# Kernel tuning notes

Hardware: AMD Instinct MI355X
Metric: run time of the kernel (lower is better)

The kernel has to match this reference:

```python
import jax, jax.numpy as jnp
import numpy as np

NUM_HEADS = 16

def setup_inputs() -> dict:
    key = jax.random.key(0)
    k1, k2, k3 = jax.random.split(key, 3)
    B, S, D = 2, 2048, 1024
    return {
        "hidden_states": jax.random.normal(k1, (B, S, D), dtype=jnp.float32),
        "W_attn": jax.random.normal(k2, (D, 3 * D), dtype=jnp.float32) * 0.02,
        "b_attn": jnp.zeros((3 * D,), dtype=jnp.float32),
        "W_proj": jax.random.normal(k3, (D, D), dtype=jnp.float32) * 0.02,
        "b_proj": jnp.zeros((D,), dtype=jnp.float32),
    }

def reference(hidden_states, W_attn, b_attn, W_proj, b_proj):
    B, S, D = hidden_states.shape
    H = NUM_HEADS
    hd = D // H
    # qkv projection (Conv1D == addmm): [B,S,3D]
    qkv = hidden_states @ W_attn + b_attn
    q, k, v = jnp.split(qkv, 3, axis=-1)
    # split heads -> [B,H,S,hd]
    def split_heads(t):
        return t.reshape(B, S, H, hd).transpose(0, 2, 1, 3)
    q, k, v = split_heads(q), split_heads(k), split_heads(v)
    # scaled QK^T: [B,H,S,S]
    scores = jnp.einsum('bhqd,bhkd->bhqk', q, k) / jnp.asarray(hd ** 0.5, dtype=q.dtype)
    causal = jnp.tril(jnp.ones((S, S), dtype=bool))
    mask_value = jnp.finfo(scores.dtype).min
    scores = jnp.where(causal, scores, mask_value)
    probs = jax.nn.softmax(scores, axis=-1)  # attn_pdrop=0 -> no dropout
    out = jnp.einsum('bhqk,bhkd->bhqd', probs, v)
    # merge heads -> [B,S,D]
    out = out.transpose(0, 2, 1, 3).reshape(B, S, D)
    out = out @ W_proj + b_proj  # resid_pdrop=0 -> no dropout
    return out
```

## Files before the change

### kernel.cpp

```cpp
#include <hip/hip_runtime.h>
#include <math.h>

typedef __attribute__((ext_vector_type(8))) short bf16x8;
typedef __attribute__((ext_vector_type(4))) short bf16x4;
typedef __attribute__((ext_vector_type(4))) float f32x4;

#define MFMA16(a, b, c) __builtin_amdgcn_mfma_f32_16x16x32_bf16(a, b, c, 0, 0, 0)

#define GLOAD_LDS16(g, l)                                                        \
    __builtin_amdgcn_global_load_lds(                                            \
        (const __attribute__((address_space(1))) void*)(g),                      \
        (__attribute__((address_space(3))) void*)(l), 16, 0, 0)

__device__ __forceinline__ short f2bf(float f) {
    union { float f; unsigned u; } x; x.f = f;
    unsigned r = (x.u + 0x7fffu + ((x.u >> 16) & 1u)) >> 16;
    return (short)r;
}

__global__ __launch_bounds__(256) void convert_bf16_kernel(
    const float* __restrict__ in, short* __restrict__ out, int n4) {
    int i = blockIdx.x * 256 + threadIdx.x;
    if (i >= n4) return;
    float4 v = ((const float4*)in)[i];
    bf16x4 o;
    o[0] = f2bf(v.x); o[1] = f2bf(v.y); o[2] = f2bf(v.z); o[3] = f2bf(v.w);
    ((bf16x4*)out)[i] = o;
}

__global__ __launch_bounds__(256) void transpose_w2_kernel(
    const float* __restrict__ Wa, const float* __restrict__ Wp,
    short* __restrict__ WaT, short* __restrict__ WpT) {
    __shared__ float tile[32][33];
    const float* W; short* Wt; int N, xb;
    if (blockIdx.x < 96) { W = Wa; Wt = WaT; N = 3072; xb = blockIdx.x; }
    else                 { W = Wp; Wt = WpT; N = 1024; xb = blockIdx.x - 96; }
    const int K = 1024;
    int c = threadIdx.x & 31, r0 = threadIdx.x >> 5;
    int n0 = xb << 5, k0 = blockIdx.y << 5;
#pragma unroll
    for (int i = 0; i < 4; i++) {
        int r = r0 + i * 8;
        tile[r][c] = W[(long)(k0 + r) * N + n0 + c];
    }
    __syncthreads();
#pragma unroll
    for (int i = 0; i < 4; i++) {
        int r = r0 + i * 8;
        Wt[(long)(n0 + r) * K + k0 + c] = f2bf(tile[c][r]);
    }
}

__global__ __launch_bounds__(256) void gemm_qkv_kernel(
    const short* __restrict__ A, const short* __restrict__ Bt,
    const float* __restrict__ bias,
    short* __restrict__ QK, short* __restrict__ VTb, int Kdim) {
    __shared__ __align__(16) short lsAll[17408];
    short* lsA = lsAll;
    short* lsB = lsAll + 8192;
    const int tid = threadIdx.x;
    const int lane = tid & 63, l15 = lane & 15, quad = lane >> 4;
    const int w = tid >> 6, wm = w >> 1, wn = w & 1;
    const int m0 = blockIdx.y * 128, n0 = blockIdx.x * 128;
    const int e = l15 & 7;
    const int lrow = lane >> 3;
    const int lgcol = ((lane & 7) ^ lrow) << 3;

    f32x4 acc[4][4];
#pragma unroll
    for (int i = 0; i < 4; i++)
#pragma unroll
        for (int j = 0; j < 4; j++) acc[i][j] = (f32x4){0.f, 0.f, 0.f, 0.f};

    for (int k0 = 0; k0 < Kdim; k0 += 64) {
#pragma unroll
        for (int ii = 0; ii < 4; ii++) {
            const int i = (w << 2) + ii;
            const int grow = (i << 3) + lrow;
            GLOAD_LDS16(&A[(size_t)(m0 + grow) * Kdim + k0 + lgcol], &lsA[i * 512]);
            GLOAD_LDS16(&Bt[(size_t)(n0 + grow) * Kdim + k0 + lgcol], &lsB[i * 512]);
        }
        __syncthreads();
#pragma unroll
        for (int kk = 0; kk < 64; kk += 32) {
            const int kb = kk >> 3;
            bf16x8 af[4], bfr[4];
#pragma unroll
            for (int t = 0; t < 4; t++) {
                const int sw = (((kb + quad) ^ e) << 3);
                af[t] = *(const bf16x8*)&lsA[(wm * 64 + t * 16 + l15) * 64 + sw];
                bfr[t] = *(const bf16x8*)&lsB[(wn * 64 + t * 16 + l15) * 64 + sw];
            }
#pragma unroll
            for (int mt = 0; mt < 4; mt++)
#pragma unroll
                for (int nt = 0; nt < 4; nt++)
                    acc[mt][nt] = MFMA16(af[mt], bfr[nt], acc[mt][nt]);
        }
        __syncthreads();
    }

    if (n0 < 2048) {
        const float scale = (n0 < 1024) ? 0.18033688011112042f : 1.0f;
#pragma unroll
        for (int nt = 0; nt < 4; nt++) {
            int nn = n0 + wn * 64 + nt * 16 + l15;
            float bv = bias[nn];
#pragma unroll
            for (int mt = 0; mt < 4; mt++)
#pragma unroll
                for (int r = 0; r < 4; r++) {
                    int mm = m0 + wm * 64 + mt * 16 + quad * 4 + r;
                    QK[(long)mm * 2048 + nn] = f2bf((acc[mt][nt][r] + bv) * scale);
                }
        }
    } else {
        short* vt = &lsAll[w * (64 * 68)];
#pragma unroll
        for (int nt = 0; nt < 4; nt++) {
            int nn = n0 + wn * 64 + nt * 16 + l15;
            float bv = bias[nn];
#pragma unroll
            for (int mt = 0; mt < 4; mt++) {
                bf16x4 pk;
#pragma unroll
                for (int r = 0; r < 4; r++) pk[r] = f2bf(acc[mt][nt][r] + bv);
                *(bf16x4*)&vt[(nt * 16 + l15) * 68 + mt * 16 + quad * 4] = pk;
            }
        }
        const int hh = ((n0 - 2048) >> 6) + wn;
        const int bb = m0 >> 11;
        const int srow = (m0 & 2047) + wm * 64;
        const int sloc = (lane & 7) << 3;
#pragma unroll
        for (int i = 0; i < 8; i++) {
            const int d = i * 8 + (lane >> 3);
            bf16x8 vv = *(const bf16x8*)&vt[d * 68 + sloc];
            *(bf16x8*)&VTb[((size_t)(bb * 16 + hh) * 64 + d) * 2048 + srow + sloc] = vv;
        }
    }
}

__global__ __launch_bounds__(256) void gemm_proj_kernel(
    const short* __restrict__ A, const short* __restrict__ Bt,
    const float* __restrict__ bias, float* __restrict__ outF) {
    __shared__ __align__(16) short lsA[128 * 64];
    __shared__ __align__(16) short lsB[64 * 64];
    const int tid = threadIdx.x;
    const int lane = tid & 63, l15 = lane & 15, quad = lane >> 4, w = tid >> 6;
    const int m0 = blockIdx.y * 128, n0 = blockIdx.x * 64;
    const int e = l15 & 7;
    const int lrow = lane >> 3;
    const int lgcol = ((lane & 7) ^ lrow) << 3;

    f32x4 acc[2][4];
#pragma unroll
    for (int i = 0; i < 2; i++)
#pragma unroll
        for (int j = 0; j < 4; j++) acc[i][j] = (f32x4){0.f, 0.f, 0.f, 0.f};

    for (int k0 = 0; k0 < 1024; k0 += 64) {
#pragma unroll
        for (int ii = 0; ii < 4; ii++) {
            const int i = (w << 2) + ii;
            const int grow = (i << 3) + lrow;
            GLOAD_LDS16(&A[(size_t)(m0 + grow) * 1024 + k0 + lgcol], &lsA[i * 512]);
        }
#pragma unroll
        for (int ii = 0; ii < 2; ii++) {
            const int i = (w << 1) + ii;
            const int grow = (i << 3) + lrow;
            GLOAD_LDS16(&Bt[(size_t)(n0 + grow) * 1024 + k0 + lgcol], &lsB[i * 512]);
        }
        __syncthreads();
#pragma unroll
        for (int kk = 0; kk < 64; kk += 32) {
            const int kb = kk >> 3;
            const int sw = (((kb + quad) ^ e) << 3);
            bf16x8 af[2], bfr[4];
#pragma unroll
            for (int mt = 0; mt < 2; mt++)
                af[mt] = *(const bf16x8*)&lsA[(w * 32 + mt * 16 + l15) * 64 + sw];
#pragma unroll
            for (int nt = 0; nt < 4; nt++)
                bfr[nt] = *(const bf16x8*)&lsB[(nt * 16 + l15) * 64 + sw];
#pragma unroll
            for (int mt = 0; mt < 2; mt++)
#pragma unroll
                for (int nt = 0; nt < 4; nt++)
                    acc[mt][nt] = MFMA16(af[mt], bfr[nt], acc[mt][nt]);
        }
        __syncthreads();
    }

#pragma unroll
    for (int nt = 0; nt < 4; nt++) {
        int nn = n0 + nt * 16 + l15;
        float bv = bias[nn];
#pragma unroll
        for (int mt = 0; mt < 2; mt++)
#pragma unroll
            for (int r = 0; r < 4; r++) {
                int mm = m0 + w * 32 + mt * 16 + quad * 4 + r;
                outF[(long)mm * 1024 + nn] = acc[mt][nt][r] + bv;
            }
    }
}

__global__ __launch_bounds__(256, 4) void attn_kernel(
    const short* __restrict__ QK, const short* __restrict__ VT,
    short* __restrict__ Ao) {
    __shared__ __align__(16) short Kt[2][64 * 64];
    __shared__ __align__(16) short Vt[2][64 * 64];
    __shared__ __align__(16) short Pt[4][1024];
    const int tid = threadIdx.x;
    const int lane = tid & 63, l15 = lane & 15, quad = lane >> 4, w = tid >> 6;
    const int bx = blockIdx.x;
    const int qt = 31 - (bx >> 5);
    const int hb = bx & 31;
    const int b = hb >> 4, h = hb & 15;
    const size_t rowbase = (size_t)b * 2048 * 2048 + h * 64;
    const short* Qb = QK + rowbase;
    const short* Kb = QK + rowbase + 1024;
    const short* Vh = VT + (size_t)hb * 64 * 2048;
    short* Pw = &Pt[w][0];
    const int e = l15 & 7;

    const int srow0 = tid >> 3, sc40 = (tid & 7) ^ (srow0 & 7);
    const int srow1 = srow0 + 32, sc41 = (tid & 7) ^ (srow1 & 7);
    const int sdst0 = srow0 * 64 + ((tid & 7) << 3);
    const int sdst1 = srow1 * 64 + ((tid & 7) << 3);

    const long qr = (long)(qt * 64 + w * 16 + l15) * 2048;
    bf16x8 qf0 = *(const bf16x8*)&Qb[qr + quad * 8];
    bf16x8 qf1 = *(const bf16x8*)&Qb[qr + 32 + quad * 8];

    float l = 0.f;
    f32x4 o[4];
#pragma unroll
    for (int dt = 0; dt < 4; dt++) o[dt] = (f32x4){0.f, 0.f, 0.f, 0.f};

    const int nc = qt + 1;

    *(bf16x8*)&Kt[0][sdst0] = *(const bf16x8*)&Kb[(size_t)srow0 * 2048 + sc40 * 8];
    *(bf16x8*)&Kt[0][sdst1] = *(const bf16x8*)&Kb[(size_t)srow1 * 2048 + sc41 * 8];
    *(bf16x8*)&Vt[0][sdst0] = *(const bf16x8*)&Vh[srow0 * 2048 + sc40 * 8];
    *(bf16x8*)&Vt[0][sdst1] = *(const bf16x8*)&Vh[srow1 * 2048 + sc41 * 8];
    __syncthreads();

    for (int c = 0; c < nc; c++) {
        const short* Kc = &Kt[c & 1][0];
        const short* Vc = &Vt[c & 1][0];
        const bool more = (c + 1 < nc);
        bf16x8 kr0, kr1, vr0, vr1;
        if (more) {
            const int k2 = (c + 1) * 64;
            kr0 = *(const bf16x8*)&Kb[(size_t)(k2 + srow0) * 2048 + sc40 * 8];
            kr1 = *(const bf16x8*)&Kb[(size_t)(k2 + srow1) * 2048 + sc41 * 8];
            vr0 = *(const bf16x8*)&Vh[srow0 * 2048 + k2 + sc40 * 8];
            vr1 = *(const bf16x8*)&Vh[srow1 * 2048 + k2 + sc41 * 8];
        }

        f32x4 s[4];
#pragma unroll
        for (int t = 0; t < 4; t++) {
            bf16x8 k0f = *(const bf16x8*)&Kc[(t * 16 + l15) * 64 + ((quad ^ e) << 3)];
            bf16x8 k1f = *(const bf16x8*)&Kc[(t * 16 + l15) * 64 + (((4 + quad) ^ e) << 3)];
            f32x4 z = (f32x4){0.f, 0.f, 0.f, 0.f};
            z = MFMA16(k0f, qf0, z);
            z = MFMA16(k1f, qf1, z);
            s[t] = z;
        }

        if (c == nc - 1) {
#pragma unroll
            for (int t = 0; t < 4; t++)
#pragma unroll
                for (int r = 0; r < 4; r++)
                    if (t * 16 + quad * 4 + r > w * 16 + l15) s[t][r] = -INFINITY;
        }

#pragma unroll
        for (int t = 0; t < 4; t++) {
            bf16x4 pw;
#pragma unroll
            for (int r = 0; r < 4; r++) {
                float pv = __builtin_amdgcn_exp2f(s[t][r]);
                l += pv;
                pw[r] = f2bf(pv);
            }
            *(bf16x4*)&Pw[l15 * 64 + (((2 * t + (quad >> 1)) ^ e) << 3) + ((quad & 1) << 2)] = pw;
        }

        bf16x8 pf0 = *(const bf16x8*)&Pw[l15 * 64 + ((quad ^ e) << 3)];
        bf16x8 pf1 = *(const bf16x8*)&Pw[l15 * 64 + (((4 + quad) ^ e) << 3)];
#pragma unroll
        for (int dt = 0; dt < 4; dt++) {
            bf16x8 v0f = *(const bf16x8*)&Vc[(dt * 16 + l15) * 64 + ((quad ^ e) << 3)];
            bf16x8 v1f = *(const bf16x8*)&Vc[(dt * 16 + l15) * 64 + (((4 + quad) ^ e) << 3)];
            o[dt] = MFMA16(v0f, pf0, o[dt]);
            o[dt] = MFMA16(v1f, pf1, o[dt]);
        }

        if (more) {
            short* Kn = &Kt[(c + 1) & 1][0];
            short* Vn = &Vt[(c + 1) & 1][0];
            *(bf16x8*)&Kn[sdst0] = kr0;
            *(bf16x8*)&Kn[sdst1] = kr1;
            *(bf16x8*)&Vn[sdst0] = vr0;
            *(bf16x8*)&Vn[sdst1] = vr1;
        }
        __syncthreads();
    }

    l += __shfl_xor(l, 16);
    l += __shfl_xor(l, 32);
    const float rl = 1.f / l;

    const int qs = qt * 64 + w * 16 + l15;
    const long base = ((long)(b * 2048 + qs)) * 1024 + h * 64;
#pragma unroll
    for (int dt = 0; dt < 4; dt++) {
        bf16x4 wv;
#pragma unroll
        for (int r = 0; r < 4; r++) wv[r] = f2bf(o[dt][r] * rl);
        *(bf16x4*)&Ao[base + dt * 16 + quad * 4] = wv;
    }
}

extern "C" void kernel_launch(void* const* d_in, const int* in_sizes, int n_in,
                              void* d_out, int out_size, void* d_ws, size_t ws_size,
                              hipStream_t stream) {
    const float* hs = (const float*)d_in[0];
    const float* W_attn = (const float*)d_in[1];
    const float* b_attn = (const float*)d_in[2];
    const float* W_proj = (const float*)d_in[3];
    const float* b_proj = (const float*)d_in[4];
    float* out = (float*)d_out;

    const size_t MB = 1024 * 1024;
    char* ws = (char*)d_ws;
    short* hs_bf = (short*)ws;
    short* attn_o = hs_bf;
    short* WaT = (short*)(ws + 8 * MB);
    short* WpT = (short*)(ws + 14 * MB);
    short* QK = (short*)(ws + 16 * MB);
    short* VTb = (short*)(ws + 32 * MB);

    convert_bf16_kernel<<<4096, 256, 0, stream>>>(hs, hs_bf, 1048576);
    transpose_w2_kernel<<<dim3(128, 32), 256, 0, stream>>>(W_attn, W_proj, WaT, WpT);
    gemm_qkv_kernel<<<dim3(24, 32), 256, 0, stream>>>(hs_bf, WaT, b_attn, QK, VTb, 1024);
    attn_kernel<<<1024, 256, 0, stream>>>(QK, VTb, attn_o);
    gemm_proj_kernel<<<dim3(16, 32), 256, 0, stream>>>(attn_o, WpT, b_proj, out);
}
```

Baseline: 181.1 us.

## Rewrite QKV GEMM with 256x256 tiles and double-buffered pipelined LDS loads

The QKV projection GEMM now uses 512-thread blocks computing 256x256 output tiles. Global-to-LDS loads for the next K tile go into a double buffer and are interleaved between MFMA phases, with explicit vmcnt waits, raw barriers and s_setprio around the MFMA bursts. The goal is to hide global memory latency and raise MFMA density per LDS read. In exchange the grid shrinks to 192 blocks, fewer than the number of CUs, and each block uses 128KB of LDS, which limits occupancy to one block per CU.

After: 167.9 us. -7.3%, faster.

```diff
diff --git a/kernel.cpp b/kernel.cpp
--- a/kernel.cpp
+++ b/kernel.cpp
@@ -51,92 +51,171 @@
     }
 }
 
-__global__ __launch_bounds__(256) void gemm_qkv_kernel(
+
+#define SBAR() __builtin_amdgcn_s_barrier()
+#define PRIO(x) __builtin_amdgcn_s_setprio(x)
+#define VMW4 asm volatile("s_waitcnt vmcnt(4)" ::: "memory")
+#define VMW2 asm volatile("s_waitcnt vmcnt(2)" ::: "memory")
+#define VMW0 asm volatile("s_waitcnt vmcnt(0)" ::: "memory")
+#define NOPS ((void)0)
+
+#define LDA8(IDX) (*(const bf16x8*)&ls[(IDX)])
+#define SA(q, k1v, nbv) GLOAD_LDS16(Ags + (size_t)(q) * 65536 + (k1v), &ls[(nbv) + (q) * 4096 + swd])
+#define SB(q, k1v, nbv) GLOAD_LDS16(Bgs + (size_t)(q) * 65536 + (k1v), &ls[(nbv) + 32768 + (q) * 4096 + swd])
+
+#define PHASE_MFMA(M0_, M1_, aa0, ba0, aa1, ba1)              \
+    PRIO(1);                                                  \
+    acc[M0_][0] = MFMA16(aa0, b00, acc[M0_][0]);              \
+    acc[M0_][1] = MFMA16(aa0, b10, acc[M0_][1]);              \
+    acc[M0_][2] = MFMA16(aa0, b20, acc[M0_][2]);              \
+    acc[M0_][3] = MFMA16(aa0, b30, acc[M0_][3]);              \
+    acc[M1_][0] = MFMA16(ba0, b00, acc[M1_][0]);              \
+    acc[M1_][1] = MFMA16(ba0, b10, acc[M1_][1]);              \
+    acc[M1_][2] = MFMA16(ba0, b20, acc[M1_][2]);              \
+    acc[M1_][3] = MFMA16(ba0, b30, acc[M1_][3]);              \
+    acc[M0_][0] = MFMA16(aa1, b01, acc[M0_][0]);              \
+    acc[M0_][1] = MFMA16(aa1, b11, acc[M0_][1]);              \
+    acc[M0_][2] = MFMA16(aa1, b21, acc[M0_][2]);              \
+    acc[M0_][3] = MFMA16(aa1, b31, acc[M0_][3]);              \
+    acc[M1_][0] = MFMA16(ba1, b01, acc[M1_][0]);              \
+    acc[M1_][1] = MFMA16(ba1, b11, acc[M1_][1]);              \
+    acc[M1_][2] = MFMA16(ba1, b21, acc[M1_][2]);              \
+    acc[M1_][3] = MFMA16(ba1, b31, acc[M1_][3]);              \
+    PRIO(0);
+
+#define KTILE(T, STG, VMP2, VMTAIL) do {                                              \
+    const int cb = ((T) & 1) << 14;                                                   \
+    const int nb = cb ^ 16384;                                                        \
+    const int k1 = ((T) + 1) << 6;                                                    \
+    (void)nb; (void)k1;                                                               \
+                                                                    \
+    if (STG) { SB(0, k1, nb); SB(1, k1, nb); }                                        \
+    const bf16x8 b00 = LDA8(cb + 32768 + bro + sw0);                                  \
+    const bf16x8 b01 = LDA8(cb + 32768 + bro + sw1);                                  \
+    const bf16x8 b10 = LDA8(cb + 32768 + bro + 1024 + sw0);                           \
+    const bf16x8 b11 = LDA8(cb + 32768 + bro + 1024 + sw1);                           \
+    const bf16x8 b20 = LDA8(cb + 32768 + bro + 2048 + sw0);                           \
+    const bf16x8 b21 = LDA8(cb + 32768 + bro + 2048 + sw1);                           \
+    const bf16x8 b30 = LDA8(cb + 32768 + bro + 3072 + sw0);                           \
+    const bf16x8 b31 = LDA8(cb + 32768 + bro + 3072 + sw1);                           \
+    {                                                                                 \
+        bf16x8 x0 = LDA8(cb + aro + sw0), x1 = LDA8(cb + aro + sw1);                  \
+        bf16x8 y0 = LDA8(cb + aro + 1024 + sw0), y1 = LDA8(cb + aro + 1024 + sw1);    \
+        SBAR();                                                                       \
+        PHASE_MFMA(0, 1, x0, y0, x1, y1)                                              \
+        SBAR();                                                                       \
+    }                                                                                 \
+                                                                    \
+    if (STG) { SB(2, k1, nb); SB(3, k1, nb); }                                        \
+    {                                                                                 \
+        bf16x8 x0 = LDA8(cb + aro + 2048 + sw0), x1 = LDA8(cb + aro + 2048 + sw1);    \
+        bf16x8 y0 = LDA8(cb + aro + 3072 + sw0), y1 = LDA8(cb + aro + 3072 + sw1);    \
+        SBAR();                                                                       \
+        PHASE_MFMA(2, 3, x0, y0, x1, y1)                                              \
+        SBAR();                                                                       \
+    }                                                                                 \
+                                                                    \
+    VMP2;                                                                             \
+    SBAR();                                                                           \
+    if (STG) { SA(0, k1, nb); SA(2, k1, nb); }                                        \
+    {                                                                                 \
+        bf16x8 x0 = LDA8(cb + aro + 4096 + sw0), x1 = LDA8(cb + aro + 4096 + sw1);    \
+        bf16x8 y0 = LDA8(cb + aro + 5120 + sw0), y1 = LDA8(cb + aro + 5120 + sw1);    \
+        PHASE_MFMA(4, 5, x0, y0, x1, y1)                                              \
+        SBAR();                                                                       \
+    }                                                                                 \
+                                                                    \
+    if (STG) { SA(1, k1, nb); SA(3, k1, nb); }                                        \
+    {                                                                                 \
+        bf16x8 x0 = LDA8(cb + aro + 6144 + sw0), x1 = LDA8(cb + aro + 6144 + sw1);    \
+        bf16x8 y0 = LDA8(cb + aro + 7168 + sw0), y1 = LDA8(cb + aro + 7168 + sw1);    \
+        SBAR();                                                                       \
+        PHASE_MFMA(6, 7, x0, y0, x1, y1)                                              \
+        VMTAIL;                                                                       \
+        SBAR();                                                                       \
+    }                                                                                 \
+} while (0)
+
+__global__ __launch_bounds__(512, 2) void gemm_qkv_kernel(
     const short* __restrict__ A, const short* __restrict__ Bt,
     const float* __restrict__ bias,
-    short* __restrict__ QK, short* __restrict__ VTb, int Kdim) {
-    __shared__ __align__(16) short lsAll[17408];
-    short* lsA = lsAll;
-    short* lsB = lsAll + 8192;
+    short* __restrict__ QK, short* __restrict__ VTb) {
+    __shared__ __align__(16) short ls[65536];
     const int tid = threadIdx.x;
     const int lane = tid & 63, l15 = lane & 15, quad = lane >> 4;
-    const int w = tid >> 6, wm = w >> 1, wn = w & 1;
-    const int m0 = blockIdx.y * 128, n0 = blockIdx.x * 128;
+    const int w = tid >> 6, wm = w >> 2, wn = w & 3;
+    const int m0 = blockIdx.y * 256, n0 = blockIdx.x * 256;
     const int e = l15 & 7;
-    const int lrow = lane >> 3;
-    const int lgcol = ((lane & 7) ^ lrow) << 3;
-
-    f32x4 acc[4][4];
-#pragma unroll
-    for (int i = 0; i < 4; i++)
+    const int sgr = (w << 3) + (lane >> 3);
+    const int sgc = ((lane & 7) ^ (lane >> 3)) << 3;
+    const int swd = w << 9;
+    const short* Ags = A + (size_t)(m0 + sgr) * 1024 + sgc;
+    const short* Bgs = Bt + (size_t)(n0 + sgr) * 1024 + sgc;
+    const int aro = (wm * 128 + l15) << 6;
+    const int bro = (wn * 64 + l15) << 6;
+    const int sw0 = (quad ^ e) << 3;
+    const int sw1 = ((4 + quad) ^ e) << 3;
+
+    f32x4 acc[8][4];
+#pragma unroll
+    for (int i = 0; i < 8; i++)
 #pragma unroll
         for (int j = 0; j < 4; j++) acc[i][j] = (f32x4){0.f, 0.f, 0.f, 0.f};
 
-    for (int k0 = 0; k0 < Kdim; k0 += 64) {
-#pragma unroll
-        for (int ii = 0; ii < 4; ii++) {
-            const int i = (w << 2) + ii;
-            const int grow = (i << 3) + lrow;
-            GLOAD_LDS16(&A[(size_t)(m0 + grow) * Kdim + k0 + lgcol], &lsA[i * 512]);
-            GLOAD_LDS16(&Bt[(size_t)(n0 + grow) * Kdim + k0 + lgcol], &lsB[i * 512]);
-        }
-        __syncthreads();
-#pragma unroll
-        for (int kk = 0; kk < 64; kk += 32) {
-            const int kb = kk >> 3;
-            bf16x8 af[4], bfr[4];
-#pragma unroll
-            for (int t = 0; t < 4; t++) {
-                const int sw = (((kb + quad) ^ e) << 3);
-                af[t] = *(const bf16x8*)&lsA[(wm * 64 + t * 16 + l15) * 64 + sw];
-                bfr[t] = *(const bf16x8*)&lsB[(wn * 64 + t * 16 + l15) * 64 + sw];
-            }
-#pragma unroll
-            for (int mt = 0; mt < 4; mt++)
-#pragma unroll
-                for (int nt = 0; nt < 4; nt++)
-                    acc[mt][nt] = MFMA16(af[mt], bfr[nt], acc[mt][nt]);
-        }
-        __syncthreads();
-    }
+    SB(0, 0, 0); SB(1, 0, 0); SB(2, 0, 0); SB(3, 0, 0);
+    SA(0, 0, 0); SA(2, 0, 0); SA(1, 0, 0); SA(3, 0, 0);
+    VMW2;
+    SBAR();
+
+#pragma unroll 2
+    for (int t = 0; t < 14; ++t) { KTILE(t, 1, VMW4, VMW2); }
+    KTILE(14, 1, VMW4, VMW0);
+    KTILE(15, 0, VMW0, NOPS);
+
+    __syncthreads();
 
     if (n0 < 2048) {
         const float scale = (n0 < 1024) ? 0.18033688011112042f : 1.0f;
 #pragma unroll
         for (int nt = 0; nt < 4; nt++) {
-            int nn = n0 + wn * 64 + nt * 16 + l15;
-            float bv = bias[nn];
-#pragma unroll
-            for (int mt = 0; mt < 4; mt++)
+            const int nn = n0 + wn * 64 + nt * 16 + l15;
+            const float bv = bias[nn];
+#pragma unroll
+            for (int mt = 0; mt < 8; mt++)
 #pragma unroll
                 for (int r = 0; r < 4; r++) {
-                    int mm = m0 + wm * 64 + mt * 16 + quad * 4 + r;
+                    const int mm = m0 + wm * 128 + mt * 16 + quad * 4 + r;
                     QK[(long)mm * 2048 + nn] = f2bf((acc[mt][nt][r] + bv) * scale);
                 }
         }
     } else {
-        short* vt = &lsAll[w * (64 * 68)];
-#pragma unroll
-        for (int nt = 0; nt < 4; nt++) {
-            int nn = n0 + wn * 64 + nt * 16 + l15;
-            float bv = bias[nn];
-#pragma unroll
-            for (int mt = 0; mt < 4; mt++) {
-                bf16x4 pk;
-#pragma unroll
-                for (int r = 0; r < 4; r++) pk[r] = f2bf(acc[mt][nt][r] + bv);
-                *(bf16x4*)&vt[(nt * 16 + l15) * 68 + mt * 16 + quad * 4] = pk;
-            }
-        }
+        short* vt = &ls[w * 4352];
         const int hh = ((n0 - 2048) >> 6) + wn;
         const int bb = m0 >> 11;
-        const int srow = (m0 & 2047) + wm * 64;
+        const int srow = (m0 & 2047) + wm * 128;
         const int sloc = (lane & 7) << 3;
 #pragma unroll
-        for (int i = 0; i < 8; i++) {
-            const int d = i * 8 + (lane >> 3);
-            bf16x8 vv = *(const bf16x8*)&vt[d * 68 + sloc];
-            *(bf16x8*)&VTb[((size_t)(bb * 16 + hh) * 64 + d) * 2048 + srow + sloc] = vv;
+        for (int half = 0; half < 2; half++) {
+#pragma unroll
+            for (int nt = 0; nt < 4; nt++) {
+                const int nn = n0 + wn * 64 + nt * 16 + l15;
+                const float bv = bias[nn];
+                const int d_ = nt * 16 + l15;
+#pragma unroll
+                for (int mt = 0; mt < 4; mt++) {
+                    const int mtg = half * 4 + mt;
+                    bf16x4 pk;
+#pragma unroll
+                    for (int r = 0; r < 4; r++) pk[r] = f2bf(acc[mtg][nt][r] + bv);
+                    *(bf16x4*)&vt[d_ * 68 + mt * 16 + quad * 4] = pk;
+                }
+            }
+#pragma unroll
+            for (int i = 0; i < 8; i++) {
+                const int d = i * 8 + (lane >> 3);
+                bf16x8 vv = *(const bf16x8*)&vt[d * 68 + sloc];
+                *(bf16x8*)&VTb[((size_t)(bb * 16 + hh) * 64 + d) * 2048 + srow + half * 64 + sloc] = vv;
+            }
         }
     }
 }
@@ -349,7 +428,7 @@
 
     convert_bf16_kernel<<<4096, 256, 0, stream>>>(hs, hs_bf, 1048576);
     transpose_w2_kernel<<<dim3(128, 32), 256, 0, stream>>>(W_attn, W_proj, WaT, WpT);
-    gemm_qkv_kernel<<<dim3(24, 32), 256, 0, stream>>>(hs_bf, WaT, b_attn, QK, VTb, 1024);
+    gemm_qkv_kernel<<<dim3(12, 16), 512, 0, stream>>>(hs_bf, WaT, b_attn, QK, VTb);
     attn_kernel<<<1024, 256, 0, stream>>>(QK, VTb, attn_o);
     gemm_proj_kernel<<<dim3(16, 32), 256, 0, stream>>>(attn_o, WpT, b_proj, out);
 }
```
